# Kernel optimization log

Hardware: AMD Instinct MI355X
Metric: run time of the kernel (lower is better)

Reference implementation:

```python
import jax, jax.numpy as jnp
import numpy as np

B, S, D, H = 2, 2048, 1024, 16
HD = D // H

def setup_inputs() -> dict:
    key = jax.random.key(0)
    ks = jax.random.split(key, 9)
    s = 1.0 / np.sqrt(D)
    inp = {"x": jax.random.normal(ks[0], (B, S, D), dtype=jnp.float32)}
    for i, name in enumerate(["q", "k", "v", "o"]):
        inp[f"W_{name}"] = jax.random.uniform(ks[1 + 2 * i], (D, D), dtype=jnp.float32, minval=-s, maxval=s)
        inp[f"b_{name}"] = jax.random.uniform(ks[2 + 2 * i], (D,), dtype=jnp.float32, minval=-s, maxval=s)
    return inp


def reference(x, W_q, b_q, W_k, b_k, W_v, b_v, W_o, b_o):
    # x: [B, S, D]
    def split_heads(t):
        return t.reshape(B, S, H, HD).transpose(0, 2, 1, 3)  # [B, H, S, HD]

    Q = split_heads(x @ W_q + b_q)
    K = split_heads(x @ W_k + b_k)
    V = split_heads(x @ W_v + b_v)

    scale = 1.0 / np.sqrt(HD).astype(np.float32)
    scores = jnp.einsum("bhqd,bhkd->bhqk", Q, K) * scale  # [B, H, S, S]
    weights = jax.nn.softmax(scores, axis=-1)
    attn = jnp.einsum("bhqk,bhkd->bhqd", weights, V)  # [B, H, S, HD]
    attn = attn.transpose(0, 2, 1, 3).reshape(B, S, D)
    return attn @ W_o + b_o
```

## Files before the change

### kernel.cpp

```cpp
#include <hip/hip_runtime.h>
#include <hip/hip_bf16.h>

#define BB 2
#define SS 2048
#define DD 1024
#define HH 16
#define HD 64

typedef __attribute__((ext_vector_type(8))) short bf16x8;
typedef __attribute__((ext_vector_type(4))) float f32x4;

__device__ __forceinline__ unsigned short f2bf(float f) {
  unsigned int u = __float_as_uint(f);
  return (unsigned short)((u + 0x7FFFu + ((u >> 16) & 1u)) >> 16);
}

__device__ __forceinline__ float fast_exp2(float x) {
#if __has_builtin(__builtin_amdgcn_exp2f)
  return __builtin_amdgcn_exp2f(x);
#else
  return __expf(x * 0.6931471805599453f);
#endif
}

__device__ __forceinline__ void async_copy16(const unsigned short* gp, unsigned short* lp) {
  __builtin_amdgcn_global_load_lds(
      (const __attribute__((address_space(1))) unsigned int*)gp,
      (__attribute__((address_space(3))) unsigned int*)lp, 16, 0, 0);
}

__device__ __forceinline__ void pl32_swap(unsigned& a, unsigned& b) {
#if __has_builtin(__builtin_amdgcn_permlane32_swap)
  auto r = __builtin_amdgcn_permlane32_swap(a, b, false, false);
  a = r[0];
  b = r[1];
#else
  asm volatile("v_permlane32_swap_b32 %0, %1" : "+v"(a), "+v"(b));
#endif
}
__device__ __forceinline__ void pl16_swap(unsigned& a, unsigned& b) {
#if __has_builtin(__builtin_amdgcn_permlane16_swap)
  auto r = __builtin_amdgcn_permlane16_swap(a, b, false, false);
  a = r[0];
  b = r[1];
#else
  asm volatile("v_permlane16_swap_b32 %0, %1" : "+v"(a), "+v"(b));
#endif
}

__global__ __launch_bounds__(256) void prep_kernel(
    const float* __restrict__ x, unsigned short* __restrict__ xb,
    const float* __restrict__ W0, unsigned short* __restrict__ T0,
    const float* __restrict__ W1, unsigned short* __restrict__ T1,
    const float* __restrict__ W2, unsigned short* __restrict__ T2,
    const float* __restrict__ W3, unsigned short* __restrict__ T3) {
  const int blk = blockIdx.x;
  const int t = threadIdx.x;
  if (blk < 4096) {
    int i = blk * 1024 + t * 4;
    float4 v = *(const float4*)(x + i);
    ushort4 u;
    u.x = f2bf(v.x); u.y = f2bf(v.y); u.z = f2bf(v.z); u.w = f2bf(v.w);
    *(ushort4*)(xb + i) = u;
    return;
  }
  const int j = blk - 4096;
  const int jw = j >> 10;
  const int tb = j & 1023;
  const float* W = jw == 0 ? W0 : (jw == 1 ? W1 : (jw == 2 ? W2 : W3));
  unsigned short* T = jw == 0 ? T0 : (jw == 1 ? T1 : (jw == 2 ? T2 : T3));
  __shared__ float tile[32][33];
  int k0 = (tb & 31) * 32, n0 = (tb >> 5) * 32;
  int c = t & 31, r0 = t >> 5;
#pragma unroll
  for (int i = 0; i < 4; ++i) {
    int r = r0 + i * 8;
    tile[r][c] = W[(size_t)(k0 + r) * DD + n0 + c];
  }
  __syncthreads();
#pragma unroll
  for (int i = 0; i < 4; ++i) {
    int r = r0 + i * 8;
    T[(size_t)(n0 + r) * DD + k0 + c] = f2bf(tile[c][r]);
  }
}

template <int STORE>
__device__ __forceinline__ void gemm_core(
    const unsigned short* __restrict__ A, const unsigned short* __restrict__ BT,
    const float* __restrict__ bias, void* __restrict__ outp, float scale,
    int bm, int bn) {
  const int t = threadIdx.x;
  const int w = t >> 6;
  const int l = t & 63;
  const int wm = (w >> 1) * 64;
  const int wn = (w & 1) * 64;

  __shared__ __align__(16) unsigned short As[128 * 32];
  __shared__ __align__(16) unsigned short Bs[128 * 32];

  f32x4 acc[4][4];
#pragma unroll
  for (int i = 0; i < 4; ++i)
#pragma unroll
    for (int j = 0; j < 4; ++j) acc[i][j] = (f32x4)0.f;

  const int fr = l & 15;
  const int kg = (l >> 4) * 8;

  for (int k0 = 0; k0 < DD; k0 += 32) {
    __syncthreads();
#pragma unroll
    for (int c = 0; c < 2; ++c) {
      int e = (w * 2 + c) * 512 + l * 8;
      int row = e >> 5, kk = e & 31;
      async_copy16(A + (size_t)(bm + row) * DD + k0 + kk, As + (w * 2 + c) * 512);
      async_copy16(BT + (size_t)(bn + row) * DD + k0 + kk, Bs + (w * 2 + c) * 512);
    }
    __syncthreads();

    bf16x8 af[4], bfr[4];
#pragma unroll
    for (int i = 0; i < 4; ++i)
      af[i] = *(const bf16x8*)(As + (wm + i * 16 + fr) * 32 + kg);
#pragma unroll
    for (int j = 0; j < 4; ++j)
      bfr[j] = *(const bf16x8*)(Bs + (wn + j * 16 + fr) * 32 + kg);
#pragma unroll
    for (int i = 0; i < 4; ++i)
#pragma unroll
      for (int j = 0; j < 4; ++j)
        acc[i][j] = __builtin_amdgcn_mfma_f32_16x16x32_bf16(af[i], bfr[j], acc[i][j], 0, 0, 0);
  }

  const int col_l = l & 15;
  const int row_l = (l >> 4) * 4;

#pragma unroll
  for (int i = 0; i < 4; ++i) {
    int m_base = bm + wm + i * 16 + row_l;
#pragma unroll
    for (int j = 0; j < 4; ++j) {
      int n = bn + wn + j * 16 + col_l;
      float bv = bias[n];
      float* out = (float*)outp;
#pragma unroll
      for (int r = 0; r < 4; ++r)
        out[(size_t)(m_base + r) * DD + n] = acc[i][j][r] + bv;
    }
  }
}

__global__ __launch_bounds__(256) void out_gemm_mfma(
    const unsigned short* __restrict__ A, const unsigned short* __restrict__ WoT,
    const float* __restrict__ bo, float* __restrict__ out) {
  const int i = blockIdx.x;
  const int xcd = i & 7;
  const int slot = i >> 3;
  const int bm = (xcd + 8 * (slot >> 3)) * 128;
  const int bn = (slot & 7) * 128;
  gemm_core<0>(A, WoT, bo, (void*)out, 1.0f, bm, bn);
}

__global__ __launch_bounds__(256, 3) void qkv_gemm_tri(
    const unsigned short* __restrict__ A,
    const unsigned short* __restrict__ WqT, const unsigned short* __restrict__ WkT,
    const unsigned short* __restrict__ WvT,
    const float* __restrict__ bq, const float* __restrict__ bk,
    const float* __restrict__ bv,
    unsigned short* __restrict__ Qo, unsigned short* __restrict__ Ko,
    unsigned short* __restrict__ VTo) {
  const int i = blockIdx.x;
  const int xcd = i & 7;
  const int slot = i >> 3;
  const int bm = (xcd + 8 * (slot / 24)) * 128;
  const int c = slot % 24;
  const int which = c >> 3;
  const int bn = (c & 7) * 128;
  const unsigned short* BT = which == 0 ? WqT : (which == 1 ? WkT : WvT);
  const float* bias = which == 0 ? bq : (which == 1 ? bk : bv);

  const int t = threadIdx.x;
  const int w = t >> 6;
  const int l = t & 63;
  const int wm = (w >> 1) * 64;
  const int wn = (w & 1) * 64;
  const int fr = l & 15;
  const int kgB = (l >> 4) * 16;

  __shared__ __align__(16) unsigned short lds[2][3][4096];

  f32x4 acc[4][4];
#pragma unroll
  for (int ii = 0; ii < 4; ++ii)
#pragma unroll
    for (int j = 0; j < 4; ++j) acc[ii][j] = (f32x4)0.f;

  int aoff[4], boff[4];
#pragma unroll
  for (int ii = 0; ii < 4; ++ii) {
    aoff[ii] = (wm + ii * 16 + fr) * 64 + kgB;
    boff[ii] = (wn + ii * 16 + fr) * 64 + kgB;
  }

  const int cc0 = w * 128 + l;
  const int cc1 = cc0 + 64;
  const int row0 = cc0 >> 2, kk0 = (cc0 & 3) * 8;
  const int row1 = cc1 >> 2, kk1 = (cc1 & 3) * 8;
  const unsigned short* a0 = A + (size_t)(bm + row0) * DD + kk0;
  const unsigned short* a1 = A + (size_t)(bm + row1) * DD + kk1;
  const unsigned short* b0 = BT + (size_t)(bn + row0) * DD + kk0;
  const unsigned short* b1 = BT + (size_t)(bn + row1) * DD + kk1;

  auto stage_tile = [&](int T) {
    if (T >= 32) return;
    const int buf = T % 3;
    const int k0 = T * 32;
    async_copy16(a0 + k0, &lds[0][buf][w * 1024]);
    async_copy16(a1 + k0, &lds[0][buf][w * 1024 + 512]);
    async_copy16(b0 + k0, &lds[1][buf][w * 1024]);
    async_copy16(b1 + k0, &lds[1][buf][w * 1024 + 512]);
  };

  auto phase = [&](int T, int vm) {
    const int buf = T % 3;
    const char* Ab = (const char*)&lds[0][buf][0];
    const char* Bb = (const char*)&lds[1][buf][0];
    bf16x8 af[4], bfr[4];
#pragma unroll
    for (int ii = 0; ii < 4; ++ii) af[ii] = *(const bf16x8*)(Ab + aoff[ii]);
#pragma unroll
    for (int j = 0; j < 4; ++j) bfr[j] = *(const bf16x8*)(Bb + boff[j]);
    stage_tile(T + 2);
    asm volatile("s_barrier" ::: "memory");
    __builtin_amdgcn_s_setprio(1);
#pragma unroll
    for (int ii = 0; ii < 4; ++ii)
#pragma unroll
      for (int j = 0; j < 4; ++j)
        acc[ii][j] = __builtin_amdgcn_mfma_f32_16x16x32_bf16(af[ii], bfr[j], acc[ii][j], 0, 0, 0);
    __builtin_amdgcn_s_setprio(0);
    if (vm == 1) asm volatile("s_waitcnt vmcnt(4)" ::: "memory");
    if (vm == 2) asm volatile("s_waitcnt vmcnt(0)" ::: "memory");
    asm volatile("s_barrier" ::: "memory");
  };

  stage_tile(0);
  stage_tile(1);
  asm volatile("s_waitcnt vmcnt(4)" ::: "memory");
  asm volatile("s_barrier" ::: "memory");

  for (int T = 0; T < 30; ++T) phase(T, 1);
  phase(30, 2);
  phase(31, 0);

  const int col_l = l & 15;
  const int row_l = (l >> 4) * 4;
  const int b_ = bm >> 11;

  if (which != 2) {
    const float scl = which == 0 ? 0.18033688011112042f : 1.0f;
    unsigned short* out = which == 0 ? Qo : Ko;
#pragma unroll
    for (int ii = 0; ii < 4; ++ii) {
      int m_base = bm + wm + ii * 16 + row_l;
#pragma unroll
      for (int j = 0; j < 4; ++j) {
        int n = bn + wn + j * 16 + col_l;
        float bv = bias[n];
        int h_ = n >> 6, hd_ = n & 63;
#pragma unroll
        for (int r = 0; r < 4; ++r) {
          int m = m_base + r;
          int b2 = m >> 11, s_ = m & 2047;
          out[(((size_t)(b2 * HH + h_) * SS) + s_) * HD + hd_] =
              f2bf((acc[ii][j][r] + bv) * scl);
        }
      }
    }
  } else {
    unsigned short* out = VTo;
    unsigned int* Tt = (unsigned int*)&lds[0][0][0];
    const int srow0 = bm & 2047;
#pragma unroll
    for (int p = 0; p < 4; ++p) {
      __syncthreads();
      if ((w & 1) == (p >> 1)) {
        const int jt0 = (p & 1) * 2;
#pragma unroll
        for (int jj = 0; jj < 2; ++jj) {
          int jt = jt0 + jj;
          int n_p = jj * 16 + col_l;
          float bv = bias[bn + p * 32 + n_p];
#pragma unroll
          for (int ii = 0; ii < 4; ++ii) {
            int m0 = wm + ii * 16 + row_l;
#pragma unroll
            for (int pr = 0; pr < 2; ++pr) {
              unsigned int val =
                  (unsigned int)f2bf(acc[ii][jt][2 * pr] + bv) |
                  ((unsigned int)f2bf(acc[ii][jt][2 * pr + 1] + bv) << 16);
              int m = m0 + 2 * pr;
              Tt[n_p * 64 + (((m >> 1)) ^ ((n_p & 7) << 2))] = val;
            }
          }
        }
      }
      __syncthreads();
#pragma unroll
      for (int cq = 0; cq < 2; ++cq) {
        int q = t + cq * 256;
        int n_p = q >> 4, cpos = q & 15;
        uint4 v = *(const uint4*)(Tt + n_p * 64 + ((cpos * 4) ^ ((n_p & 7) << 2)));
        int n_glob = bn + p * 32 + n_p;
        int h_ = n_glob >> 6, hd_ = n_glob & 63;
        *(uint4*)(out + ((size_t)((b_ * HH + h_) * HD + hd_)) * SS + srow0 + cpos * 8) = v;
      }
    }
  }
}

__global__ __launch_bounds__(512, 4) void flash_attn_mfma(
    const unsigned short* __restrict__ Q,
    const unsigned short* __restrict__ K,
    const unsigned short* __restrict__ VT,
    unsigned short* __restrict__ ctx) {
  const int bh = blockIdx.x;
  const int qt = blockIdx.y;
  const int b  = bh >> 4;
  const int h  = bh & 15;
  const int t  = threadIdx.x;
  const int w  = t >> 6;
  const int l  = t & 63;
  const int wg = w & 3;
  const int wh = w >> 2;
  const int g  = l >> 4;
  const int ln = l & 15;

  const unsigned short* Qp = Q + ((size_t)bh * SS + (size_t)qt * 64 + wg * 16) * HD;
  const unsigned short* Kp = K + (size_t)bh * SS * HD;
  const unsigned short* Vp = VT + (size_t)bh * HD * SS;

  __shared__ __align__(16) unsigned short smem[2][2][2][2048];
  __shared__ __align__(16) float rred[4 * 64];

  bf16x8 qf[2];
#pragma unroll
  for (int kb = 0; kb < 2; ++kb)
    qf[kb] = *(const bf16x8*)(Qp + ln * HD + kb * 32 + g * 8);

  f32x4 o[4];
#pragma unroll
  for (int mt = 0; mt < 4; ++mt) o[mt] = (f32x4)0.f;
  float rs = 0.f;

  const int sp  = w >> 2;
  const int sq  = w & 3;
  const int idx = sq * 64 + l;
  const int rowK = idx >> 3;
  const int gccK = (idx & 7) ^ (rowK & 7);
  const unsigned short* kgp = Kp + (size_t)(sp * 32 + rowK) * HD + gccK * 8;
  const int rowV = idx >> 2;
  const int gc2V = (idx & 3) ^ ((rowV >> 1) & 3);
  const unsigned short* vgp = Vp + (size_t)rowV * SS + sp * 32 + gc2V * 8;
  unsigned short* dK = &smem[0][sp][0][sq * 512];
  unsigned short* dV = &smem[1][sp][0][sq * 512];

  int ko[2][2];
#pragma unroll
  for (int kb = 0; kb < 2; ++kb)
#pragma unroll
    for (int mt = 0; mt < 2; ++mt) {
      int row = mt * 16 + ln;
      ko[kb][mt] = row * 128 + (((kb * 4 + g) ^ (row & 7)) * 16);
    }
  int vo[4];
#pragma unroll
  for (int mt = 0; mt < 4; ++mt) {
    int row = mt * 16 + ln;
    vo[mt] = row * 64 + ((g ^ ((row >> 1) & 3)) * 16);
  }
  const char* kpar = (const char*)&smem[0][wh][0][0];
  const char* vpar = (const char*)&smem[1][wh][0][0];

  auto stage_i = [&](int db) {
    async_copy16(kgp, dK + db * 2048);
    async_copy16(vgp, dV + db * 2048);
    kgp += 64 * HD;
    vgp += 64;
  };

  auto body = [&](int db) {
    const char* Kst = kpar + db * 4096;
    const char* Vst = vpar + db * 4096;

    f32x4 st[2];
#pragma unroll
    for (int mt = 0; mt < 2; ++mt) st[mt] = (f32x4)0.f;
#pragma unroll
    for (int kb = 0; kb < 2; ++kb)
#pragma unroll
      for (int mt = 0; mt < 2; ++mt) {
        bf16x8 ka = *(const bf16x8*)(Kst + ko[kb][mt]);
        st[mt] = __builtin_amdgcn_mfma_f32_16x16x32_bf16(ka, qf[kb], st[mt], 0, 0, 0);
      }

    unsigned Sd[2][2];
#pragma unroll
    for (int mt = 0; mt < 2; ++mt) {
      float p0 = fast_exp2(st[mt][0]);
      float p1 = fast_exp2(st[mt][1]);
      float p2 = fast_exp2(st[mt][2]);
      float p3 = fast_exp2(st[mt][3]);
      Sd[mt][0] = __builtin_amdgcn_perm(__float_as_uint(p1), __float_as_uint(p0),
                                        0x07060302u);
      Sd[mt][1] = __builtin_amdgcn_perm(__float_as_uint(p3), __float_as_uint(p2),
                                        0x07060302u);
      rs += (p0 + p1) + (p2 + p3);
    }
#pragma unroll
    for (int p = 0; p < 2; ++p) pl32_swap(Sd[0][p], Sd[1][p]);
#pragma unroll
    for (int p = 0; p < 2; ++p) pl16_swap(Sd[0][p], Sd[1][p]);

    bf16x8 pbv;
    {
      union { unsigned u[4]; bf16x8 v; } cu;
      cu.u[0] = Sd[0][0];
      cu.u[1] = Sd[0][1];
      cu.u[2] = Sd[1][0];
      cu.u[3] = Sd[1][1];
      pbv = cu.v;
    }
#pragma unroll
    for (int mt = 0; mt < 4; ++mt) {
      bf16x8 va = *(const bf16x8*)(Vst + vo[mt]);
      o[mt] = __builtin_amdgcn_mfma_f32_16x16x32_bf16(va, pbv, o[mt], 0, 0, 0);
    }
  };

  stage_i(0);
  for (int kt2 = 0; kt2 < 16; ++kt2) {
    __syncthreads();
    stage_i(1);
    body(0);
    __syncthreads();
    if (kt2 < 15) stage_i(0);
    body(1);
  }

  __syncthreads();
  {
    float* ored = (float*)&smem[0][0][0][0];
    float* rb = ored + (wg * 64 + l) * 16;
    float* sb = rred + wg * 64 + l;
    if (wh == 1) {
#pragma unroll
      for (int mt = 0; mt < 4; ++mt)
        *(f32x4*)(rb + ((unsigned)(mt ^ (l & 3)) * 4)) = o[mt];
      sb[0] = rs;
    }
    __syncthreads();
    if (wh == 1) return;
#pragma unroll
    for (int mt = 0; mt < 4; ++mt) {
      f32x4 pv = *(const f32x4*)(rb + ((unsigned)(mt ^ (l & 3)) * 4));
      o[mt] += pv;
    }
    rs += sb[0];
  }

  {
    float lsum = rs;
    lsum += __shfl_xor(lsum, 16, 64);
    lsum += __shfl_xor(lsum, 32, 64);
    float inv = 1.f / lsum;
    int srow = qt * 64 + wg * 16 + ln;
    unsigned short* cb = ctx + (size_t)(b * SS + srow) * DD + h * HD;
#pragma unroll
    for (int mt = 0; mt < 4; ++mt) {
      ushort4 u4;
      u4.x = f2bf(o[mt][0] * inv);
      u4.y = f2bf(o[mt][1] * inv);
      u4.z = f2bf(o[mt][2] * inv);
      u4.w = f2bf(o[mt][3] * inv);
      *(ushort4*)(cb + mt * 16 + 4 * g) = u4;
    }
  }
}

extern "C" void kernel_launch(void* const* d_in, const int* in_sizes, int n_in,
                              void* d_out, int out_size, void* d_ws, size_t ws_size,
                              hipStream_t stream) {
  const float* x  = (const float*)d_in[0];
  const float* Wq = (const float*)d_in[1];
  const float* bq = (const float*)d_in[2];
  const float* Wk = (const float*)d_in[3];
  const float* bk = (const float*)d_in[4];
  const float* Wv = (const float*)d_in[5];
  const float* bv = (const float*)d_in[6];
  const float* Wo = (const float*)d_in[7];
  const float* bo = (const float*)d_in[8];
  float* out = (float*)d_out;

  const size_t ELEMS = (size_t)BB * SS * DD;
  char* ws = (char*)d_ws;
  unsigned short* xb   = (unsigned short*)ws;  ws += ELEMS * 2;
  unsigned short* WqT  = (unsigned short*)ws;  ws += (size_t)DD * DD * 2;
  unsigned short* WkT  = (unsigned short*)ws;  ws += (size_t)DD * DD * 2;
  unsigned short* WvT  = (unsigned short*)ws;  ws += (size_t)DD * DD * 2;
  unsigned short* WoT  = (unsigned short*)ws;  ws += (size_t)DD * DD * 2;
  unsigned short* Qb   = (unsigned short*)ws;  ws += ELEMS * 2;
  unsigned short* Kb   = (unsigned short*)ws;  ws += ELEMS * 2;
  unsigned short* VbT  = (unsigned short*)ws;  ws += ELEMS * 2;
  unsigned short* ctxb = (unsigned short*)ws;  ws += ELEMS * 2;

  prep_kernel<<<8192, 256, 0, stream>>>(x, xb, Wq, WqT, Wk, WkT, Wv, WvT, Wo, WoT);

  qkv_gemm_tri<<<768, 256, 0, stream>>>(xb, WqT, WkT, WvT, bq, bk, bv,
                                        Qb, Kb, VbT);

  dim3 attn_grid(BB * HH, SS / 64);
  flash_attn_mfma<<<attn_grid, 512, 0, stream>>>(Qb, Kb, VbT, ctxb);

  out_gemm_mfma<<<256, 256, 0, stream>>>(ctxb, WoT, bo, out);
}
```

Before: 193.7 us.

## Process two query sub-tiles per wave in flash attention to reuse K/V fragments

Each wave now handles 32 query rows (two 16-row MFMA tiles) instead of 16, so each K and V fragment read from LDS feeds two MFMAs. The query tile per block doubles to 128 and the grid halves. Launch bounds drop to 2 blocks per CU to make room for the doubled accumulators. The aim is to cut LDS traffic and global K/V staging per query row, at the cost of more registers and fewer blocks (512), which may hurt occupancy and load balance across CUs.

```diff
diff --git a/kernel.cpp b/kernel.cpp
--- a/kernel.cpp
+++ b/kernel.cpp
@@ -320,7 +320,7 @@
   }
 }
 
-__global__ __launch_bounds__(512, 4) void flash_attn_mfma(
+__global__ __launch_bounds__(512, 2) void flash_attn_mfma(
     const unsigned short* __restrict__ Q,
     const unsigned short* __restrict__ K,
     const unsigned short* __restrict__ VT,
@@ -337,22 +337,26 @@
   const int g  = l >> 4;
   const int ln = l & 15;
 
-  const unsigned short* Qp = Q + ((size_t)bh * SS + (size_t)qt * 64 + wg * 16) * HD;
+  const unsigned short* Qp = Q + ((size_t)bh * SS + (size_t)qt * 128 + wg * 32) * HD;
   const unsigned short* Kp = K + (size_t)bh * SS * HD;
   const unsigned short* Vp = VT + (size_t)bh * HD * SS;
 
   __shared__ __align__(16) unsigned short smem[2][2][2][2048];
-  __shared__ __align__(16) float rred[4 * 64];
-
-  bf16x8 qf[2];
-#pragma unroll
-  for (int kb = 0; kb < 2; ++kb)
-    qf[kb] = *(const bf16x8*)(Qp + ln * HD + kb * 32 + g * 8);
-
-  f32x4 o[4];
-#pragma unroll
-  for (int mt = 0; mt < 4; ++mt) o[mt] = (f32x4)0.f;
-  float rs = 0.f;
+  __shared__ __align__(16) float rred[4 * 64 * 2];
+
+  bf16x8 qf[2][2];
+#pragma unroll
+  for (int nt = 0; nt < 2; ++nt)
+#pragma unroll
+    for (int kb = 0; kb < 2; ++kb)
+      qf[nt][kb] = *(const bf16x8*)(Qp + (nt * 16 + ln) * HD + kb * 32 + g * 8);
+
+  f32x4 o[2][4];
+#pragma unroll
+  for (int nt = 0; nt < 2; ++nt)
+#pragma unroll
+    for (int mt = 0; mt < 4; ++mt) o[nt][mt] = (f32x4)0.f;
+  float rs[2] = {0.f, 0.f};
 
   const int sp  = w >> 2;
   const int sq  = w & 3;
@@ -394,48 +398,56 @@
     const char* Kst = kpar + db * 4096;
     const char* Vst = vpar + db * 4096;
 
-    f32x4 st[2];
-#pragma unroll
-    for (int mt = 0; mt < 2; ++mt) st[mt] = (f32x4)0.f;
+    f32x4 st[2][2];
+#pragma unroll
+    for (int nt = 0; nt < 2; ++nt)
+#pragma unroll
+      for (int mt = 0; mt < 2; ++mt) st[nt][mt] = (f32x4)0.f;
 #pragma unroll
     for (int kb = 0; kb < 2; ++kb)
 #pragma unroll
       for (int mt = 0; mt < 2; ++mt) {
         bf16x8 ka = *(const bf16x8*)(Kst + ko[kb][mt]);
-        st[mt] = __builtin_amdgcn_mfma_f32_16x16x32_bf16(ka, qf[kb], st[mt], 0, 0, 0);
+        st[0][mt] = __builtin_amdgcn_mfma_f32_16x16x32_bf16(ka, qf[0][kb], st[0][mt], 0, 0, 0);
+        st[1][mt] = __builtin_amdgcn_mfma_f32_16x16x32_bf16(ka, qf[1][kb], st[1][mt], 0, 0, 0);
       }
 
-    unsigned Sd[2][2];
-#pragma unroll
-    for (int mt = 0; mt < 2; ++mt) {
-      float p0 = fast_exp2(st[mt][0]);
-      float p1 = fast_exp2(st[mt][1]);
-      float p2 = fast_exp2(st[mt][2]);
-      float p3 = fast_exp2(st[mt][3]);
-      Sd[mt][0] = __builtin_amdgcn_perm(__float_as_uint(p1), __float_as_uint(p0),
-                                        0x07060302u);
-      Sd[mt][1] = __builtin_amdgcn_perm(__float_as_uint(p3), __float_as_uint(p2),
-                                        0x07060302u);
-      rs += (p0 + p1) + (p2 + p3);
-    }
-#pragma unroll
-    for (int p = 0; p < 2; ++p) pl32_swap(Sd[0][p], Sd[1][p]);
-#pragma unroll
-    for (int p = 0; p < 2; ++p) pl16_swap(Sd[0][p], Sd[1][p]);
-
-    bf16x8 pbv;
-    {
+    unsigned Sd[2][2][2];
+#pragma unroll
+    for (int nt = 0; nt < 2; ++nt) {
+#pragma unroll
+      for (int mt = 0; mt < 2; ++mt) {
+        float p0 = fast_exp2(st[nt][mt][0]);
+        float p1 = fast_exp2(st[nt][mt][1]);
+        float p2 = fast_exp2(st[nt][mt][2]);
+        float p3 = fast_exp2(st[nt][mt][3]);
+        Sd[nt][mt][0] = __builtin_amdgcn_perm(__float_as_uint(p1), __float_as_uint(p0),
+                                              0x07060302u);
+        Sd[nt][mt][1] = __builtin_amdgcn_perm(__float_as_uint(p3), __float_as_uint(p2),
+                                              0x07060302u);
+        rs[nt] += (p0 + p1) + (p2 + p3);
+      }
+#pragma unroll
+      for (int p = 0; p < 2; ++p) pl32_swap(Sd[nt][0][p], Sd[nt][1][p]);
+#pragma unroll
+      for (int p = 0; p < 2; ++p) pl16_swap(Sd[nt][0][p], Sd[nt][1][p]);
+    }
+
+    bf16x8 pbv[2];
+#pragma unroll
+    for (int nt = 0; nt < 2; ++nt) {
       union { unsigned u[4]; bf16x8 v; } cu;
-      cu.u[0] = Sd[0][0];
-      cu.u[1] = Sd[0][1];
-      cu.u[2] = Sd[1][0];
-      cu.u[3] = Sd[1][1];
-      pbv = cu.v;
+      cu.u[0] = Sd[nt][0][0];
+      cu.u[1] = Sd[nt][0][1];
+      cu.u[2] = Sd[nt][1][0];
+      cu.u[3] = Sd[nt][1][1];
+      pbv[nt] = cu.v;
     }
 #pragma unroll
     for (int mt = 0; mt < 4; ++mt) {
       bf16x8 va = *(const bf16x8*)(Vst + vo[mt]);
-      o[mt] = __builtin_amdgcn_mfma_f32_16x16x32_bf16(va, pbv, o[mt], 0, 0, 0);
+      o[0][mt] = __builtin_amdgcn_mfma_f32_16x16x32_bf16(va, pbv[0], o[0][mt], 0, 0, 0);
+      o[1][mt] = __builtin_amdgcn_mfma_f32_16x16x32_bf16(va, pbv[1], o[1][mt], 0, 0, 0);
     }
   };
 
@@ -452,38 +464,48 @@
   __syncthreads();
   {
     float* ored = (float*)&smem[0][0][0][0];
-    float* rb = ored + (wg * 64 + l) * 16;
-    float* sb = rred + wg * 64 + l;
+    float* rb = ored + (wg * 64 + l) * 32;
+    float* sb = rred + (wg * 64 + l) * 2;
     if (wh == 1) {
 #pragma unroll
-      for (int mt = 0; mt < 4; ++mt)
-        *(f32x4*)(rb + ((unsigned)(mt ^ (l & 3)) * 4)) = o[mt];
-      sb[0] = rs;
+      for (int nt = 0; nt < 2; ++nt)
+#pragma unroll
+        for (int mt = 0; mt < 4; ++mt) {
+          int idx2 = nt * 4 + mt;
+          *(f32x4*)(rb + ((unsigned)(idx2 ^ (l & 7)) * 4)) = o[nt][mt];
+        }
+      sb[0] = rs[0];
+      sb[1] = rs[1];
     }
     __syncthreads();
     if (wh == 1) return;
 #pragma unroll
-    for (int mt = 0; mt < 4; ++mt) {
-      f32x4 pv = *(const f32x4*)(rb + ((unsigned)(mt ^ (l & 3)) * 4));
-      o[mt] += pv;
-    }
-    rs += sb[0];
-  }
-
-  {
-    float lsum = rs;
+    for (int nt = 0; nt < 2; ++nt)
+#pragma unroll
+      for (int mt = 0; mt < 4; ++mt) {
+        int idx2 = nt * 4 + mt;
+        f32x4 pv = *(const f32x4*)(rb + ((unsigned)(idx2 ^ (l & 7)) * 4));
+        o[nt][mt] += pv;
+      }
+    rs[0] += sb[0];
+    rs[1] += sb[1];
+  }
+
+#pragma unroll
+  for (int nt = 0; nt < 2; ++nt) {
+    float lsum = rs[nt];
     lsum += __shfl_xor(lsum, 16, 64);
     lsum += __shfl_xor(lsum, 32, 64);
     float inv = 1.f / lsum;
-    int srow = qt * 64 + wg * 16 + ln;
+    int srow = qt * 128 + wg * 32 + nt * 16 + ln;
     unsigned short* cb = ctx + (size_t)(b * SS + srow) * DD + h * HD;
 #pragma unroll
     for (int mt = 0; mt < 4; ++mt) {
       ushort4 u4;
-      u4.x = f2bf(o[mt][0] * inv);
-      u4.y = f2bf(o[mt][1] * inv);
-      u4.z = f2bf(o[mt][2] * inv);
-      u4.w = f2bf(o[mt][3] * inv);
+      u4.x = f2bf(o[nt][mt][0] * inv);
+      u4.y = f2bf(o[nt][mt][1] * inv);
+      u4.z = f2bf(o[nt][mt][2] * inv);
+      u4.w = f2bf(o[nt][mt][3] * inv);
       *(ushort4*)(cb + mt * 16 + 4 * g) = u4;
     }
   }
@@ -520,7 +542,7 @@
   qkv_gemm_tri<<<768, 256, 0, stream>>>(xb, WqT, WkT, WvT, bq, bk, bv,
                                         Qb, Kb, VbT);
 
-  dim3 attn_grid(BB * HH, SS / 64);
+  dim3 attn_grid(BB * HH, SS / 128);
   flash_attn_mfma<<<attn_grid, 512, 0, stream>>>(Qb, Kb, VbT, ctxb);
 
   out_gemm_mfma<<<256, 256, 0, stream>>>(ctxb, WoT, bo, out);
```

Result: faster. 185.4 us (-4.3%).
